# Kernel tuning notes

Hardware: AMD Instinct MI355X
Metric: run time of the kernel (lower is better)

The kernel has to match this reference:

```python
import jax, jax.numpy as jnp
import numpy as np

N, E, IN_DIM, HEADS, OUT_DIM = 50000, 800000, 256, 4, 32
NEG_SLOPE = 0.2

def setup_inputs() -> dict:
    key = jax.random.key(0)
    k1, k2, k3, k4, k5 = jax.random.split(key, 5)
    x = jax.random.normal(k1, (N, IN_DIM), dtype=jnp.float32)
    edge_index = jax.random.randint(k2, (2, E), 0, N, dtype=jnp.int64)
    s = 1.0 / np.sqrt(IN_DIM)
    W_l = jax.random.normal(k3, (IN_DIM, HEADS * OUT_DIM), dtype=jnp.float32) * s
    W_r = jax.random.normal(k4, (IN_DIM, HEADS * OUT_DIM), dtype=jnp.float32) * s
    att = jax.random.normal(k5, (HEADS, OUT_DIM), dtype=jnp.float32) * (1.0 / np.sqrt(OUT_DIM))
    bias = jnp.zeros((HEADS * OUT_DIM,), dtype=jnp.float32)
    return {"x": x, "edge_index": edge_index, "W_l": W_l, "W_r": W_r, "att": att, "bias": bias}

def reference(x, edge_index, W_l, W_r, att, bias):
    n = x.shape[0]
    # add self loops (PyG GATv2Conv default add_self_loops=True)
    loops = jnp.arange(n, dtype=edge_index.dtype)
    src = jnp.concatenate([edge_index[0], loops])  # message sources j
    dst = jnp.concatenate([edge_index[1], loops])  # message targets i
    xl = (x @ W_l).reshape(n, HEADS, OUT_DIM)  # source-side features
    xr = (x @ W_r).reshape(n, HEADS, OUT_DIM)  # target-side features
    # GATv2 score: a^T LeakyReLU(W_l h_j + W_r h_i), per head
    e = jax.nn.leaky_relu(xl[src] + xr[dst], NEG_SLOPE)  # [Etot,H,C]
    logits = jnp.einsum('ehc,hc->eh', e, att)  # [Etot,H]
    # segment softmax over incoming edges per destination node
    m = jax.ops.segment_max(logits, dst, num_segments=n)  # [N,H]
    ex = jnp.exp(logits - m[dst])
    denom = jax.ops.segment_sum(ex, dst, num_segments=n)  # [N,H]
    alpha = ex / (denom[dst] + 1e-16)  # [Etot,H]
    # scatter-add weighted source features
    out = jax.ops.segment_sum(alpha[:, :, None] * xl[src], dst, num_segments=n)  # [N,H,C]
    out = out.reshape(n, HEADS * OUT_DIM) + bias
    return jax.nn.relu(out)
```

## Files before the change

kernel.cpp:

```cpp
#include <hip/hip_runtime.h>
#include <math.h>

typedef unsigned short ushort_t;
typedef unsigned int uint_t;
typedef __attribute__((ext_vector_type(8))) short short8;
typedef __attribute__((ext_vector_type(4))) float f32x4;

#define MAXDEG 64
#define BUCKCAP 8192

__device__ __forceinline__ ushort_t f2bf(float f) {
  uint_t x = __float_as_uint(f);
  uint_t r = (x + 0x7fffu + ((x >> 16) & 1u)) >> 16;
  return (ushort_t)r;
}
__device__ __forceinline__ float bflo(uint_t u) { return __uint_as_float(u << 16); }
__device__ __forceinline__ float bfhi(uint_t u) { return __uint_as_float(u & 0xffff0000u); }

__global__ __launch_bounds__(256) void prep_wt(const float* __restrict__ Wl,
                                               const float* __restrict__ Wr,
                                               ushort_t* __restrict__ wt,
                                               int* __restrict__ tails) {
  int gi = blockIdx.x * 256 + threadIdx.x;
  int kc = gi >> 11;
  int rem = gi & 2047;
  int nn = rem >> 3;
  int k8 = rem & 7;
  const float* W = (nn < 128) ? Wl : Wr;
  int col = nn & 127;
  short8 v;
#pragma unroll
  for (int e = 0; e < 8; ++e) {
    int k = kc * 64 + k8 * 8 + e;
    v[e] = (short)f2bf(W[(size_t)k * 128 + col]);
  }
  int dstg = kc * 2048 + nn * 8 + (k8 ^ (nn & 7));
  *reinterpret_cast<short8*>(wt + (size_t)dstg * 8) = v;
  if (gi < 256) tails[gi] = 0;
}

__global__ __launch_bounds__(512) void gemm_fullB(
    const float* __restrict__ x, const ushort_t* __restrict__ wt,
    ushort_t* __restrict__ xlb, ushort_t* __restrict__ xrb, int n) {
  __shared__ ushort_t bs[256 * 256];
  const int tid = threadIdx.x;
#pragma unroll
  for (int i = 0; i < 16; ++i) {
    int f = i * 512 + tid;
    __builtin_amdgcn_global_load_lds(
        (const __attribute__((address_space(1))) unsigned int*)(wt + (size_t)f * 8),
        (__attribute__((address_space(3))) unsigned int*)&bs[f * 8], 16, 0, 0);
  }
  __syncthreads();

  const int lane = tid & 63;
  const int wv = tid >> 6;
  const int l15 = lane & 15;
  const int g = lane >> 4;
  const int klane = g * 8;
  const int nstrips = (n + 15) >> 4;
  const int sstep = gridDim.x * 8;

  float4 xa[8], xb[8], na[8], nb[8];
#define XLOAD(A, B, ss)                                                     \
  {                                                                         \
    int row_ = (ss)*16 + l15;                                               \
    int rowc_ = (row_ < n) ? row_ : (n - 1);                                \
    const float* xr_ = x + (size_t)rowc_ * 256;                             \
    _Pragma("unroll") for (int kt = 0; kt < 8; ++kt) {                      \
      A[kt] = *reinterpret_cast<const float4*>(xr_ + kt * 32 + klane);      \
      B[kt] = *reinterpret_cast<const float4*>(xr_ + kt * 32 + klane + 4);  \
    }                                                                       \
  }

  int s = blockIdx.x * 8 + wv;
  if (s < nstrips) XLOAD(xa, xb, s);
  for (; s < nstrips; s += sstep) {
    if (s + sstep < nstrips) XLOAD(na, nb, s + sstep);

    f32x4 acc[16];
#pragma unroll
    for (int ct = 0; ct < 16; ++ct) acc[ct] = (f32x4)(0.f);

#pragma unroll
    for (int kt = 0; kt < 8; ++kt) {
      short8 a;
      a[0] = (short)f2bf(xa[kt].x); a[1] = (short)f2bf(xa[kt].y);
      a[2] = (short)f2bf(xa[kt].z); a[3] = (short)f2bf(xa[kt].w);
      a[4] = (short)f2bf(xb[kt].x); a[5] = (short)f2bf(xb[kt].y);
      a[6] = (short)f2bf(xb[kt].z); a[7] = (short)f2bf(xb[kt].w);
      const int kc = kt >> 1;
      const int c8 = (kt & 1) * 4 + g;
#pragma unroll
      for (int ct = 0; ct < 16; ++ct) {
        int rr = ct * 16 + l15;
        short8 b = *reinterpret_cast<const short8*>(
            &bs[kc * 16384 + rr * 64 + ((c8 ^ (rr & 7)) * 8)]);
        acc[ct] = __builtin_amdgcn_mfma_f32_16x16x32_bf16(a, b, acc[ct], 0, 0, 0);
      }
    }

    const int r0 = s * 16;
    const int rowb = r0 + g * 4;
    if (r0 + 16 <= n) {
#pragma unroll
      for (int ct = 0; ct < 8; ++ct) {
        int col = ct * 16 + l15;
#pragma unroll
        for (int j = 0; j < 4; ++j)
          xlb[(size_t)(rowb + j) * 128 + col] = f2bf(acc[ct][j]);
      }
#pragma unroll
      for (int ct = 8; ct < 16; ++ct) {
        int col = ct * 16 + l15 - 128;
#pragma unroll
        for (int j = 0; j < 4; ++j)
          xrb[(size_t)(rowb + j) * 128 + col] = f2bf(acc[ct][j]);
      }
    } else {
#pragma unroll
      for (int ct = 0; ct < 8; ++ct) {
        int col = ct * 16 + l15;
#pragma unroll
        for (int j = 0; j < 4; ++j) {
          int r = rowb + j;
          if (r < n) xlb[(size_t)r * 128 + col] = f2bf(acc[ct][j]);
        }
      }
#pragma unroll
      for (int ct = 8; ct < 16; ++ct) {
        int col = ct * 16 + l15 - 128;
#pragma unroll
        for (int j = 0; j < 4; ++j) {
          int r = rowb + j;
          if (r < n) xrb[(size_t)r * 128 + col] = f2bf(acc[ct][j]);
        }
      }
    }
#pragma unroll
    for (int kt = 0; kt < 8; ++kt) { xa[kt] = na[kt]; xb[kt] = nb[kt]; }
  }
#undef XLOAD
}

__global__ __launch_bounds__(256) void bin_edges(const int* __restrict__ ei,
                                                 uint_t* __restrict__ pairbuf,
                                                 int* __restrict__ tails, int E) {
  __shared__ int hist[256];
  __shared__ int off[256];
  const int tid = threadIdx.x;
  hist[tid] = 0;
  __syncthreads();
  const int base_e = blockIdx.x * 4096;
  uint_t pr[16];
  int bn[16];
#pragma unroll
  for (int j = 0; j < 16; ++j) {
    int e = base_e + j * 256 + tid;
    if (e < E) {
      int d = ei[E + e];
      int s = ei[e];
      pr[j] = ((uint_t)d << 16) | (uint_t)(s & 0xffff);
      bn[j] = d >> 8;
      atomicAdd(&hist[bn[j]], 1);
    } else {
      bn[j] = -1;
    }
  }
  __syncthreads();
  {
    int h = hist[tid];
    off[tid] = (h > 0) ? atomicAdd(&tails[tid], h) : 0;
  }
  __syncthreads();
#pragma unroll
  for (int j = 0; j < 16; ++j) {
    if (bn[j] >= 0) {
      int p = atomicAdd(&off[bn[j]], 1);
      if (p < BUCKCAP) pairbuf[(size_t)bn[j] * BUCKCAP + p] = pr[j];
    }
  }
}

__global__ __launch_bounds__(512) void fine_fill(const uint_t* __restrict__ pairbuf,
                                                 const int* __restrict__ tails,
                                                 int* __restrict__ cursor,
                                                 ushort_t* __restrict__ csr, int n) {
  __shared__ int cnt[256];
  const int b = blockIdx.x;
  const int lo = b << 8;
  const int tid = threadIdx.x;
  if (tid < 256) cnt[tid] = 0;
  __syncthreads();
  int tot = tails[b];
  tot = (tot < BUCKCAP) ? tot : BUCKCAP;
  const uint_t* __restrict__ pb = pairbuf + (size_t)b * BUCKCAP;
  for (int i = tid; i < tot; i += 512) {
    uint_t pr = pb[i];
    int d = pr >> 16;
    int s = pr & 0xffffu;
    int p = atomicAdd(&cnt[d - lo], 1);
    if (p < MAXDEG) csr[(size_t)d * MAXDEG + p] = (ushort_t)s;
  }
  __syncthreads();
  if (tid < 256) {
    int v = lo + tid;
    if (v < n) cursor[v] = cnt[tid];
  }
}

__global__ __launch_bounds__(256) void gat_main(
    const ushort_t* __restrict__ xlb, const ushort_t* __restrict__ xrb,
    const ushort_t* __restrict__ csr, const int* __restrict__ cursor,
    const float* __restrict__ att, const float* __restrict__ bias,
    float* __restrict__ out, int n) {
  const int tid = threadIdx.x;
  const int lane = tid & 63;
  const int ln = lane & 31;
  const int i = blockIdx.x * 8 + (tid >> 6) * 2 + (lane >> 5);
  const bool alive = (i < n);
  const int ic = alive ? i : (n - 1);
  const int nm1 = n - 1;

  const float4 att4 = reinterpret_cast<const float4*>(att)[ln];
  const float4 b4 = reinterpret_cast<const float4*>(bias)[ln];
  const uint2* __restrict__ xl4 = reinterpret_cast<const uint2*>(xlb);
  const uint2* __restrict__ xr2 = reinterpret_cast<const uint2*>(xrb);
  uint2 xu = xr2[(size_t)ic * 32 + ln];
  float4 xr4;
  xr4.x = bflo(xu.x); xr4.y = bfhi(xu.x); xr4.z = bflo(xu.y); xr4.w = bfhi(xu.y);

  const int e0 = ic * MAXDEG;

  uint2 nv[8], nv2[8];
#define LOADB(buf, bb)                                                  \
  {                                                                     \
    int eb_ = e0 + (bb)*8;                                              \
    _Pragma("unroll") for (int j = 0; j < 8; ++j) {                     \
      int sj = (int)csr[eb_ + j];                                       \
      sj = (sj < nm1) ? sj : nm1;                                       \
      buf[j] = xl4[(size_t)sj * 32 + ln];                               \
    }                                                                   \
  }
  LOADB(nv, 0);
  LOADB(nv2, 1);

  uint2 su = xl4[(size_t)ic * 32 + ln];
  float sv0 = bflo(su.x), sv1 = bfhi(su.x), sv2 = bflo(su.y), sv3 = bfhi(su.y);
  float z, part;
  z = sv0 + xr4.x; part = att4.x * fmaxf(z, 0.2f * z);
  z = sv1 + xr4.y; part = fmaf(att4.y, fmaxf(z, 0.2f * z), part);
  z = sv2 + xr4.z; part = fmaf(att4.z, fmaxf(z, 0.2f * z), part);
  z = sv3 + xr4.w; part = fmaf(att4.w, fmaxf(z, 0.2f * z), part);
  part += __shfl_xor(part, 4);
  part += __shfl_xor(part, 2);
  part += __shfl_xor(part, 1);
  const float m = part;
  float psA = 0.0f, psB = 0.0f;
  float a0A = sv0, a1A = sv1, a2A = sv2, a3A = sv3;
  float a0B = 0.f, a1B = 0.f, a2B = 0.f, a3B = 0.f;

  int deg = cursor[ic];
  deg = (deg < MAXDEG) ? deg : MAXDEG;
  const int nb8 = (deg + 7) >> 3;
  int nbw = nb8;
  { int o = __shfl_xor(nb8, 32); nbw = (o > nbw) ? o : nbw; }

  for (int b = 0; b < nbw; ++b) {
    float v0j[8], v1j[8], v2j[8], v3j[8];
#pragma unroll
    for (int j = 0; j < 8; ++j) {
      v0j[j] = bflo(nv[j].x); v1j[j] = bfhi(nv[j].x);
      v2j[j] = bflo(nv[j].y); v3j[j] = bfhi(nv[j].y);
      nv[j] = nv2[j];
    }
    if (b + 2 < nbw) LOADB(nv2, b + 2);
    const int limit = deg - b * 8;
    float a[8];
#pragma unroll
    for (int j = 0; j < 8; ++j) {
      float z0 = v0j[j] + xr4.x, z1 = v1j[j] + xr4.y;
      float z2 = v2j[j] + xr4.z, z3 = v3j[j] + xr4.w;
      float aj = att4.x * fmaxf(z0, 0.2f * z0);
      aj = fmaf(att4.y, fmaxf(z1, 0.2f * z1), aj);
      aj = fmaf(att4.z, fmaxf(z2, 0.2f * z2), aj);
      aj = fmaf(att4.w, fmaxf(z3, 0.2f * z3), aj);
      a[j] = (j < limit) ? aj : -1e30f;
    }
#pragma unroll
    for (int j = 0; j < 8; ++j) a[j] += __shfl_xor(a[j], 4);
    float t0 = (lane & 4) ? a[1] : a[0];
    float t1 = (lane & 4) ? a[3] : a[2];
    float t2 = (lane & 4) ? a[5] : a[4];
    float t3 = (lane & 4) ? a[7] : a[6];
    t0 += __shfl_xor(t0, 2);
    t1 += __shfl_xor(t1, 2);
    t2 += __shfl_xor(t2, 2);
    t3 += __shfl_xor(t3, 2);
    float u0 = (lane & 2) ? t1 : t0;
    float u1 = (lane & 2) ? t3 : t2;
    u0 += __shfl_xor(u0, 1);
    u1 += __shfl_xor(u1, 1);
    float d = (lane & 1) ? u1 : u0;
    float p = __expf(d - m);
    const int basel = lane & 56;
    float p0 = __shfl(p, basel + 0);
    float p1 = __shfl(p, basel + 4);
    float p2 = __shfl(p, basel + 2);
    float p3 = __shfl(p, basel + 6);
    float p4 = __shfl(p, basel + 1);
    float p5 = __shfl(p, basel + 5);
    float p6 = __shfl(p, basel + 3);
    float p7 = __shfl(p, basel + 7);
    if (b & 1) {
      a0B += p0 * v0j[0] + p1 * v0j[1] + p2 * v0j[2] + p3 * v0j[3] +
             p4 * v0j[4] + p5 * v0j[5] + p6 * v0j[6] + p7 * v0j[7];
      a1B += p0 * v1j[0] + p1 * v1j[1] + p2 * v1j[2] + p3 * v1j[3] +
             p4 * v1j[4] + p5 * v1j[5] + p6 * v1j[6] + p7 * v1j[7];
      a2B += p0 * v2j[0] + p1 * v2j[1] + p2 * v2j[2] + p3 * v2j[3] +
             p4 * v2j[4] + p5 * v2j[5] + p6 * v2j[6] + p7 * v2j[7];
      a3B += p0 * v3j[0] + p1 * v3j[1] + p2 * v3j[2] + p3 * v3j[3] +
             p4 * v3j[4] + p5 * v3j[5] + p6 * v3j[6] + p7 * v3j[7];
      psB += p;
    } else {
      a0A += p0 * v0j[0] + p1 * v0j[1] + p2 * v0j[2] + p3 * v0j[3] +
             p4 * v0j[4] + p5 * v0j[5] + p6 * v0j[6] + p7 * v0j[7];
      a1A += p0 * v1j[0] + p1 * v1j[1] + p2 * v1j[2] + p3 * v1j[3] +
             p4 * v1j[4] + p5 * v1j[5] + p6 * v1j[6] + p7 * v1j[7];
      a2A += p0 * v2j[0] + p1 * v2j[1] + p2 * v2j[2] + p3 * v2j[3] +
             p4 * v2j[4] + p5 * v2j[5] + p6 * v2j[6] + p7 * v2j[7];
      a3A += p0 * v3j[0] + p1 * v3j[1] + p2 * v3j[2] + p3 * v3j[3] +
             p4 * v3j[4] + p5 * v3j[5] + p6 * v3j[6] + p7 * v3j[7];
      psA += p;
    }
  }
#undef LOADB
  float ps = psA + psB;
  ps += __shfl_xor(ps, 4);
  ps += __shfl_xor(ps, 2);
  ps += __shfl_xor(ps, 1);
  float s = 1.0f + ps;
  float inv = 1.0f / (s + 1e-16f);
  if (alive) {
    float4 o;
    o.x = fmaxf(fmaf(a0A + a0B, inv, b4.x), 0.0f);
    o.y = fmaxf(fmaf(a1A + a1B, inv, b4.y), 0.0f);
    o.z = fmaxf(fmaf(a2A + a2B, inv, b4.z), 0.0f);
    o.w = fmaxf(fmaf(a3A + a3B, inv, b4.w), 0.0f);
    reinterpret_cast<float4*>(out)[(size_t)i * 32 + ln] = o;
  }
}

extern "C" void kernel_launch(void* const* d_in, const int* in_sizes, int n_in,
                              void* d_out, int out_size, void* d_ws, size_t ws_size,
                              hipStream_t stream) {
  const float* x    = (const float*)d_in[0];
  const int*   ei   = (const int*)d_in[1];
  const float* Wl   = (const float*)d_in[2];
  const float* Wr   = (const float*)d_in[3];
  const float* att  = (const float*)d_in[4];
  const float* bias = (const float*)d_in[5];
  float* out = (float*)d_out;
  const int n = in_sizes[0] / 256;
  const int E = in_sizes[1] / 2;
  const int NB = (n + 255) >> 8;

  ushort_t* xlb   = (ushort_t*)d_ws;
  ushort_t* xrb   = xlb + (size_t)n * 128;
  int* cursor     = (int*)(xrb + (size_t)n * 128);
  ushort_t* csr   = (ushort_t*)(cursor + n);
  ushort_t* wt    = csr + (size_t)n * MAXDEG;
  int* tails      = (int*)(wt + 256 * 256);
  uint_t* pairbuf = (uint_t*)(tails + 256);

  prep_wt<<<32, 256, 0, stream>>>(Wl, Wr, wt, tails);
  gemm_fullB<<<256, 512, 0, stream>>>(x, wt, xlb, xrb, n);
  bin_edges<<<(E + 4095) / 4096, 256, 0, stream>>>(ei, pairbuf, tails, E);
  fine_fill<<<NB, 512, 0, stream>>>(pairbuf, tails, cursor, csr, n);
  gat_main<<<(n + 7) / 8, 256, 0, stream>>>(xlb, xrb, csr, cursor, att, bias, out, n);
}
```

Baseline: 95.77 us.

## Merge independent preprocessing kernels to overlap weight prep with edge binning and GEMM with CSR fill

Weight conversion and edge binning now run in one launch, distinguished by block index, and the GEMM and fine CSR fill share a second launch. The aim is fewer kernel launches and letting the independent graph-preprocessing work run alongside the dense stages instead of serially. The tails reset moves to a memset, which adds one small operation. The GEMM blocks use a lot of LDS (128KB), so the fill blocks may be co-scheduled only on leftover CUs.

```diff
diff --git a/kernel.cpp b/kernel.cpp
--- a/kernel.cpp
+++ b/kernel.cpp
@@ -17,33 +17,96 @@
 __device__ __forceinline__ float bflo(uint_t u) { return __uint_as_float(u << 16); }
 __device__ __forceinline__ float bfhi(uint_t u) { return __uint_as_float(u & 0xffff0000u); }
 
-__global__ __launch_bounds__(256) void prep_wt(const float* __restrict__ Wl,
-                                               const float* __restrict__ Wr,
-                                               ushort_t* __restrict__ wt,
-                                               int* __restrict__ tails) {
-  int gi = blockIdx.x * 256 + threadIdx.x;
-  int kc = gi >> 11;
-  int rem = gi & 2047;
-  int nn = rem >> 3;
-  int k8 = rem & 7;
-  const float* W = (nn < 128) ? Wl : Wr;
-  int col = nn & 127;
-  short8 v;
-#pragma unroll
-  for (int e = 0; e < 8; ++e) {
-    int k = kc * 64 + k8 * 8 + e;
-    v[e] = (short)f2bf(W[(size_t)k * 128 + col]);
-  }
-  int dstg = kc * 2048 + nn * 8 + (k8 ^ (nn & 7));
-  *reinterpret_cast<short8*>(wt + (size_t)dstg * 8) = v;
-  if (gi < 256) tails[gi] = 0;
-}
-
-__global__ __launch_bounds__(512) void gemm_fullB(
+__global__ __launch_bounds__(256) void prep_bin(
+    const float* __restrict__ Wl, const float* __restrict__ Wr,
+    ushort_t* __restrict__ wt, const int* __restrict__ ei,
+    uint_t* __restrict__ pairbuf, int* __restrict__ tails, int E) {
+  const int tid = threadIdx.x;
+  if (blockIdx.x < 32) {
+    int gi = blockIdx.x * 256 + tid;
+    int kc = gi >> 11;
+    int rem = gi & 2047;
+    int nn = rem >> 3;
+    int k8 = rem & 7;
+    const float* W = (nn < 128) ? Wl : Wr;
+    int col = nn & 127;
+    short8 v;
+#pragma unroll
+    for (int e = 0; e < 8; ++e) {
+      int k = kc * 64 + k8 * 8 + e;
+      v[e] = (short)f2bf(W[(size_t)k * 128 + col]);
+    }
+    int dstg = kc * 2048 + nn * 8 + (k8 ^ (nn & 7));
+    *reinterpret_cast<short8*>(wt + (size_t)dstg * 8) = v;
+    return;
+  }
+  __shared__ int hist[256];
+  __shared__ int off[256];
+  hist[tid] = 0;
+  __syncthreads();
+  const int base_e = (blockIdx.x - 32) * 4096;
+  uint_t pr[16];
+  int bn[16];
+#pragma unroll
+  for (int j = 0; j < 16; ++j) {
+    int e = base_e + j * 256 + tid;
+    if (e < E) {
+      int d = ei[E + e];
+      int s = ei[e];
+      pr[j] = ((uint_t)d << 16) | (uint_t)(s & 0xffff);
+      bn[j] = d >> 8;
+      atomicAdd(&hist[bn[j]], 1);
+    } else {
+      bn[j] = -1;
+    }
+  }
+  __syncthreads();
+  {
+    int h = hist[tid];
+    off[tid] = (h > 0) ? atomicAdd(&tails[tid], h) : 0;
+  }
+  __syncthreads();
+#pragma unroll
+  for (int j = 0; j < 16; ++j) {
+    if (bn[j] >= 0) {
+      int p = atomicAdd(&off[bn[j]], 1);
+      if (p < BUCKCAP) pairbuf[(size_t)bn[j] * BUCKCAP + p] = pr[j];
+    }
+  }
+}
+
+__global__ __launch_bounds__(512) void gemm_fine(
     const float* __restrict__ x, const ushort_t* __restrict__ wt,
-    ushort_t* __restrict__ xlb, ushort_t* __restrict__ xrb, int n) {
+    ushort_t* __restrict__ xlb, ushort_t* __restrict__ xrb, int n,
+    const uint_t* __restrict__ pairbuf, const int* __restrict__ tails,
+    int* __restrict__ cursor, ushort_t* __restrict__ csr) {
+  const int tid = threadIdx.x;
+
+  if ((int)blockIdx.x >= 256) {
+    __shared__ int cnt[256];
+    const int b = blockIdx.x - 256;
+    const int lo = b << 8;
+    if (tid < 256) cnt[tid] = 0;
+    __syncthreads();
+    int tot = tails[b];
+    tot = (tot < BUCKCAP) ? tot : BUCKCAP;
+    const uint_t* __restrict__ pb = pairbuf + (size_t)b * BUCKCAP;
+    for (int i = tid; i < tot; i += 512) {
+      uint_t pr = pb[i];
+      int d = pr >> 16;
+      int s = pr & 0xffffu;
+      int p = atomicAdd(&cnt[d - lo], 1);
+      if (p < MAXDEG) csr[(size_t)d * MAXDEG + p] = (ushort_t)s;
+    }
+    __syncthreads();
+    if (tid < 256) {
+      int v = lo + tid;
+      if (v < n) cursor[v] = cnt[tid];
+    }
+    return;
+  }
+
   __shared__ ushort_t bs[256 * 256];
-  const int tid = threadIdx.x;
 #pragma unroll
   for (int i = 0; i < 16; ++i) {
     int f = i * 512 + tid;
@@ -59,7 +122,7 @@
   const int g = lane >> 4;
   const int klane = g * 8;
   const int nstrips = (n + 15) >> 4;
-  const int sstep = gridDim.x * 8;
+  const int sstep = 256 * 8;
 
   float4 xa[8], xb[8], na[8], nb[8];
 #define XLOAD(A, B, ss)                                                     \
@@ -141,72 +204,6 @@
     for (int kt = 0; kt < 8; ++kt) { xa[kt] = na[kt]; xb[kt] = nb[kt]; }
   }
 #undef XLOAD
-}
-
-__global__ __launch_bounds__(256) void bin_edges(const int* __restrict__ ei,
-                                                 uint_t* __restrict__ pairbuf,
-                                                 int* __restrict__ tails, int E) {
-  __shared__ int hist[256];
-  __shared__ int off[256];
-  const int tid = threadIdx.x;
-  hist[tid] = 0;
-  __syncthreads();
-  const int base_e = blockIdx.x * 4096;
-  uint_t pr[16];
-  int bn[16];
-#pragma unroll
-  for (int j = 0; j < 16; ++j) {
-    int e = base_e + j * 256 + tid;
-    if (e < E) {
-      int d = ei[E + e];
-      int s = ei[e];
-      pr[j] = ((uint_t)d << 16) | (uint_t)(s & 0xffff);
-      bn[j] = d >> 8;
-      atomicAdd(&hist[bn[j]], 1);
-    } else {
-      bn[j] = -1;
-    }
-  }
-  __syncthreads();
-  {
-    int h = hist[tid];
-    off[tid] = (h > 0) ? atomicAdd(&tails[tid], h) : 0;
-  }
-  __syncthreads();
-#pragma unroll
-  for (int j = 0; j < 16; ++j) {
-    if (bn[j] >= 0) {
-      int p = atomicAdd(&off[bn[j]], 1);
-      if (p < BUCKCAP) pairbuf[(size_t)bn[j] * BUCKCAP + p] = pr[j];
-    }
-  }
-}
-
-__global__ __launch_bounds__(512) void fine_fill(const uint_t* __restrict__ pairbuf,
-                                                 const int* __restrict__ tails,
-                                                 int* __restrict__ cursor,
-                                                 ushort_t* __restrict__ csr, int n) {
-  __shared__ int cnt[256];
-  const int b = blockIdx.x;
-  const int lo = b << 8;
-  const int tid = threadIdx.x;
-  if (tid < 256) cnt[tid] = 0;
-  __syncthreads();
-  int tot = tails[b];
-  tot = (tot < BUCKCAP) ? tot : BUCKCAP;
-  const uint_t* __restrict__ pb = pairbuf + (size_t)b * BUCKCAP;
-  for (int i = tid; i < tot; i += 512) {
-    uint_t pr = pb[i];
-    int d = pr >> 16;
-    int s = pr & 0xffffu;
-    int p = atomicAdd(&cnt[d - lo], 1);
-    if (p < MAXDEG) csr[(size_t)d * MAXDEG + p] = (ushort_t)s;
-  }
-  __syncthreads();
-  if (tid < 256) {
-    int v = lo + tid;
-    if (v < n) cursor[v] = cnt[tid];
-  }
 }
 
 __global__ __launch_bounds__(256) void gat_main(
@@ -373,9 +370,9 @@
   int* tails      = (int*)(wt + 256 * 256);
   uint_t* pairbuf = (uint_t*)(tails + 256);
 
-  prep_wt<<<32, 256, 0, stream>>>(Wl, Wr, wt, tails);
-  gemm_fullB<<<256, 512, 0, stream>>>(x, wt, xlb, xrb, n);
-  bin_edges<<<(E + 4095) / 4096, 256, 0, stream>>>(ei, pairbuf, tails, E);
-  fine_fill<<<NB, 512, 0, stream>>>(pairbuf, tails, cursor, csr, n);
+  hipMemsetAsync(tails, 0, 256 * sizeof(int), stream);
+  const int binb = (E + 4095) / 4096;
+  prep_bin<<<32 + binb, 256, 0, stream>>>(Wl, Wr, wt, ei, pairbuf, tails, E);
+  gemm_fine<<<256 + NB, 512, 0, stream>>>(x, wt, xlb, xrb, n, pairbuf, tails, cursor, csr);
   gat_main<<<(n + 7) / 8, 256, 0, stream>>>(xlb, xrb, csr, cursor, att, bias, out, n);
 }
```

Result: faster. 91.58 us (median of 2 runs) (-4.4%).
